# Kernel optimization log

Measured on AMD Instinct MI355X. Metric: run time of the kernel, lower is better.

## Reference

```python
import jax, jax.numpy as jnp
import numpy as np

B, GNN_DIM, TR_DIM, F = 16384, 512, 768, 1024


def setup_inputs() -> dict:
    key = jax.random.key(0)
    ks = jax.random.split(key, 16)
    s = 0.02
    return {
        "gnn_features": jax.random.normal(ks[0], (B, GNN_DIM), jnp.float32),
        "transformer_features": jax.random.normal(ks[1], (B, TR_DIM), jnp.float32),
        # gnn_projector / transformer_projector (torch Linear: y = x @ W.T + b)
        "Wg": jax.random.normal(ks[2], (F, GNN_DIM), jnp.float32) * s,
        "bg": jnp.zeros((F,), jnp.float32),
        "Wt": jax.random.normal(ks[3], (F, TR_DIM), jnp.float32) * s,
        "bt": jnp.zeros((F,), jnp.float32),
        # MultiheadAttention value-projection slice of in_proj_weight and out_proj.
        # With seq_len==1 the softmax over a single key is identically 1, so the
        # attention output is exactly out_proj(v_proj(key)); Q/K projections do
        # not affect the output (their gradients are exactly zero).
        "Wv": jax.random.normal(ks[4], (F, F), jnp.float32) * s,
        "bv": jnp.zeros((F,), jnp.float32),
        "Wo": jax.random.normal(ks[5], (F, F), jnp.float32) * s,
        "bo": jnp.zeros((F,), jnp.float32),
        # fusion_layers: Linear(2F -> F), GELU, Dropout(eval: identity), Linear(F -> F)
        "W1": jax.random.normal(ks[6], (F, 2 * F), jnp.float32) * s,
        "b1": jnp.zeros((F,), jnp.float32),
        "W2": jax.random.normal(ks[7], (F, F), jnp.float32) * s,
        "b2": jnp.zeros((F,), jnp.float32),
    }


def reference(gnn_features, transformer_features, Wg, bg, Wt, bt, Wv, bv, Wo, bo, W1, b1, W2, b2):
    # projections to fusion space  [B, F]
    gnn_proj = gnn_features @ Wg.T + bg
    tr_proj = transformer_features @ Wt.T + bt
    # degenerate single-token cross-attention: softmax over 1 key == 1, so
    # attn(q, k, v=k) = out_proj(v_proj(k)) regardless of the query.
    gnn_attended = (tr_proj @ Wv.T + bv) @ Wo.T + bo   # attention(gnn_seq, tr_seq, tr_seq)
    tr_attended = (gnn_proj @ Wv.T + bv) @ Wo.T + bo   # attention(tr_seq, gnn_seq, gnn_seq)
    combined = jnp.concatenate([gnn_attended, tr_attended], axis=-1)  # [B, 2F]
    h = jax.nn.gelu(combined @ W1.T + b1, approximate=False)          # exact GELU (torch default)
    fused = h @ W2.T + b2
    return fused + gnn_proj + tr_proj
```

## Files before the change

kernel.cpp:

```cpp
#include <hip/hip_runtime.h>
#include <cmath>

#define GAS __attribute__((address_space(1)))
#define LAS __attribute__((address_space(3)))

typedef __bf16 bf16x8 __attribute__((ext_vector_type(8)));
typedef float f32x4 __attribute__((ext_vector_type(4)));
typedef float f32x16 __attribute__((ext_vector_type(16)));

__device__ __forceinline__ void gload16(const void* g, void* l) {
    __builtin_amdgcn_global_load_lds((const GAS void*)g, (LAS void*)l, 16, 0, 0);
}

__global__ void k_prep(const float* __restrict__ gnn, const float* __restrict__ tr,
                       const float* __restrict__ Wo, const float* __restrict__ W1,
                       const float* __restrict__ W2, const float* __restrict__ Wg,
                       const float* __restrict__ Wt, const float* __restrict__ Wv,
                       __bf16* __restrict__ X, __bf16* __restrict__ W1ab,
                       __bf16* __restrict__ Wp, __bf16* __restrict__ Wv_b,
                       __bf16* __restrict__ WoT, __bf16* __restrict__ WgT,
                       __bf16* __restrict__ WtT) {
    __shared__ float t[32][33];
    int b = blockIdx.x;
    int tid = threadIdx.x;
    if (b < 12928) {
        const float* src; __bf16* dst; int sld, dld, base, c8;
        if (b < 4096)       { src=gnn;     sld=512;  dst=X+1024;         dld=2304; base=0;     c8=64; }
        else if (b < 10240) { src=tr;      sld=768;  dst=X+1536;         dld=2304; base=4096;  c8=96; }
        else if (b < 10752) { src=W1;      sld=2048; dst=W1ab;           dld=1024; base=10240; c8=128; }
        else if (b < 11264) { src=W1+1024; sld=2048; dst=W1ab+1024*1024; dld=1024; base=10752; c8=128; }
        else if (b < 11776) { src=W2;      sld=1024; dst=Wp;             dld=2304; base=11264; c8=128; }
        else if (b < 12032) { src=Wg;      sld=512;  dst=Wp+1024;        dld=2304; base=11776; c8=64; }
        else if (b < 12416) { src=Wt;      sld=768;  dst=Wp+1536;       dld=2304; base=12032; c8=96; }
        else                { src=Wv;      sld=1024; dst=Wv_b;           dld=1024; base=12416; c8=128; }
        int idx = (b - base) * 256 + tid;
        int r = idx / c8;
        int c = (idx - r * c8) << 3;
        const float4* s = reinterpret_cast<const float4*>(src + (long)r * sld + c);
        float4 x0 = s[0], x1 = s[1];
        bf16x8 v;
        v[0]=(__bf16)x0.x; v[1]=(__bf16)x0.y; v[2]=(__bf16)x0.z; v[3]=(__bf16)x0.w;
        v[4]=(__bf16)x1.x; v[5]=(__bf16)x1.y; v[6]=(__bf16)x1.z; v[7]=(__bf16)x1.w;
        *reinterpret_cast<bf16x8*>(dst + (long)r * dld + c) = v;
    } else {
        int bb = b - 12928;
        const float* src; __bf16* dst; int R, C, tile;
        if (bb < 1024)      { src=Wo; dst=WoT; R=1024; C=1024; tile=bb; }
        else if (bb < 1536) { src=Wg; dst=WgT; R=1024; C=512;  tile=bb-1024; }
        else                { src=Wt; dst=WtT; R=1024; C=768;  tile=bb-1536; }
        int tx_n = C >> 5;
        int c0 = (tile % tx_n) << 5, r0 = (tile / tx_n) << 5;
        int tx = tid & 31, ty = tid >> 5;
        #pragma unroll
        for (int i = 0; i < 32; i += 8)
            t[ty + i][tx] = src[(long)(r0 + ty + i) * C + c0 + tx];
        __syncthreads();
        #pragma unroll
        for (int i = 0; i < 32; i += 8)
            dst[(long)(c0 + ty + i) * R + r0 + tx] = (__bf16)t[tx][ty + i];
    }
}

__global__ void k_bias1(const float* __restrict__ Wo, const float* __restrict__ bv,
                        const float* __restrict__ bo, const float* __restrict__ Wv,
                        const float* __restrict__ bt, const float* __restrict__ bg,
                        float* __restrict__ b_att, float* __restrict__ vb_t,
                        float* __restrict__ vb_g) {
    int b = blockIdx.x;
    const float* mat; const float* vec; float* dst; int i; bool addbo = false;
    if (b < 1024)      { mat = Wo; vec = bv; dst = b_att; i = b;        addbo = true; }
    else if (b < 2048) { mat = Wv; vec = bt; dst = vb_t;  i = b - 1024; }
    else               { mat = Wv; vec = bg; dst = vb_g;  i = b - 2048; }
    float s = 0.f;
    for (int k = threadIdx.x; k < 1024; k += 256) s += mat[(long)i * 1024 + k] * vec[k];
    __shared__ float red[256];
    red[threadIdx.x] = s;
    __syncthreads();
    for (int off = 128; off > 0; off >>= 1) {
        if (threadIdx.x < off) red[threadIdx.x] += red[threadIdx.x + off];
        __syncthreads();
    }
    if (threadIdx.x == 0) dst[i] = red[0] + (addbo ? bo[i] : 0.f);
}

__global__ void k_bias_z2(const float* __restrict__ W1, const float* __restrict__ b_att,
                          const float* __restrict__ b1, const __bf16* __restrict__ U12,
                          const float* __restrict__ vb_t, const float* __restrict__ vb_g,
                          const float* __restrict__ bt, const float* __restrict__ bg,
                          const float* __restrict__ b2,
                          float* __restrict__ bz2, float* __restrict__ b_out) {
    int i = blockIdx.x;
    float s = 0.f;
    for (int k = threadIdx.x; k < 1024; k += 256) {
        s += (W1[(long)i * 2048 + k] + W1[(long)i * 2048 + 1024 + k]) * b_att[k];
        s += (float)U12[(long)i * 1024 + k] * vb_t[k];
        s += (float)U12[(long)(i + 1024) * 1024 + k] * vb_g[k];
    }
    __shared__ float red[256];
    red[threadIdx.x] = s;
    __syncthreads();
    for (int off = 128; off > 0; off >>= 1) {
        if (threadIdx.x < off) red[threadIdx.x] += red[threadIdx.x + off];
        __syncthreads();
    }
    if (threadIdx.x == 0) {
        bz2[i] = red[0] + b1[i];
        b_out[i] = b2[i] + bg[i] + bt[i];
    }
}

__device__ __forceinline__ void gemm64_body(
    const __bf16* __restrict__ A, int lda,
    const __bf16* __restrict__ B, int ldb,
    __bf16* __restrict__ C, int ldc,
    int K, int n_tiles, int bid) {
    constexpr int BM = 64, BN = 64, BK = 32;
    constexpr int MR = 2, NR = 2;
    __shared__ alignas(16) __bf16 As[2][BM][BK];
    __shared__ alignas(16) __bf16 Bs[2][BN][BK];

    const int tid = threadIdx.x;
    const int lane = tid & 63;
    const int wave = tid >> 6;
    const int bn = bid % n_tiles;
    const int bm = bid / n_tiles;
    const int m0 = bm * BM, n0 = bn * BN;

    const int rp_l = tid >> 2;
    const int sp = tid & 3;
    const int wr = (wave >> 1) * 32;
    const int wc = (wave & 1) * 32;
    const int fr = lane & 15;
    const int fb = (lane >> 4) << 4;

    f32x4 acc[MR][NR] = {};
    const int nk = K / BK;

    auto stage = [&](int buf, int kt) {
        int rl = (rp_l & ~1) | ((rp_l ^ (rp_l >> 2)) & 1);
        int sl = sp ^ (rl & 3);
        gload16(A + (long)(m0 + rl) * lda + kt * BK + sl * 8, (char*)&As[buf][0][0] + tid * 16);
        gload16(B + (long)(n0 + rl) * ldb + kt * BK + sl * 8, (char*)&Bs[buf][0][0] + tid * 16);
    };

    stage(0, 0);
    for (int kt = 0; kt < nk; ++kt) {
        const int buf = kt & 1;
        __syncthreads();
        if (kt + 1 < nk) stage(buf ^ 1, kt + 1);
        const char* abase = (const char*)&As[buf][0][0];
        const char* bbase = (const char*)&Bs[buf][0][0];
        bf16x8 af[MR], bfr[NR];
        #pragma unroll
        for (int m = 0; m < MR; ++m) {
            int r = wr + m * 16 + fr;
            af[m] = *(const bf16x8*)(abase + (((r << 6) + fb) ^ ((r & 7) << 4)));
        }
        #pragma unroll
        for (int n = 0; n < NR; ++n) {
            int r = wc + n * 16 + fr;
            bfr[n] = *(const bf16x8*)(bbase + (((r << 6) + fb) ^ ((r & 7) << 4)));
        }
        #pragma unroll
        for (int m = 0; m < MR; ++m)
            #pragma unroll
            for (int n = 0; n < NR; ++n)
                acc[m][n] = __builtin_amdgcn_mfma_f32_16x16x32_bf16(af[m], bfr[n], acc[m][n], 0, 0, 0);
    }

    const int r0 = (lane >> 4) << 2;
    #pragma unroll
    for (int n = 0; n < NR; ++n) {
        const int gc = n0 + wc + n * 16 + fr;
        #pragma unroll
        for (int m = 0; m < MR; ++m) {
            const long rbase = (long)(m0 + wr + m * 16 + r0);
            #pragma unroll
            for (int r = 0; r < 4; ++r)
                C[(rbase + r) * ldc + gc] = (__bf16)acc[m][n][r];
        }
    }
}

__global__ __launch_bounds__(256, 2) void k_gemmL1(
    const __bf16* __restrict__ W1ab, const __bf16* __restrict__ WoT,
    const __bf16* __restrict__ WtT, const __bf16* __restrict__ WgT,
    const __bf16* __restrict__ Wv_b, __bf16* __restrict__ U12,
    __bf16* __restrict__ VtT, __bf16* __restrict__ VgT) {
    int b = blockIdx.x;
    if (b < 512)      gemm64_body(W1ab, 1024, WoT, 1024, U12, 1024, 1024, 16, b);
    else if (b < 704) gemm64_body(WtT, 1024, Wv_b, 1024, VtT, 1024, 1024, 16, b - 512);
    else              gemm64_body(WgT, 1024, Wv_b, 1024, VgT, 1024, 1024, 16, b - 704);
}

__global__ __launch_bounds__(256, 2) void k_gemmL2(
    const __bf16* __restrict__ U12, const __bf16* __restrict__ VtT,
    const __bf16* __restrict__ VgT, __bf16* __restrict__ M1) {
    int b = blockIdx.x;
    if (b < 192) gemm64_body(U12, 1024, VtT, 1024, M1 + 512, 1280, 1024, 12, b);
    else         gemm64_body(U12 + 1024 * 1024, 1024, VgT, 1024, M1, 1280, 1024, 8, b - 192);
}

template <int MODE>
__device__ __forceinline__ void gemm8_body(
    const __bf16* __restrict__ A, int lda,
    const __bf16* __restrict__ B, int ldb,
    void* __restrict__ Cv, int ldc,
    const float* __restrict__ bias,
    int K, int n_tiles) {
    __shared__ char lds[131072];

    const int tid = threadIdx.x;
    const int lane = tid & 63;
    const int wave = tid >> 6;
    const int wm = wave >> 2;
    const int wn = wave & 3;

    int bid = blockIdx.x;
    const int nwg = gridDim.x;
    if ((nwg & 7) == 0) bid = (bid & 7) * (nwg >> 3) + (bid >> 3);
    const int bn = bid % n_tiles;
    const int bm = bid / n_tiles;
    const int m0 = bm * 256, n0 = bn * 256;

    const int rowA = ((tid >> 7) << 4) + (tid & 15);
    const int colA = (((tid >> 6) & 1) << 5) + (((tid >> 4) & 3) << 3);
    const int rowB = ((tid >> 6) << 4) + (tid & 15);
    const int colB = (((tid >> 4) & 3) << 3);
    const __bf16* Ag = A + (long)(m0 + rowA) * lda + colA;
    const __bf16* Bg = B + (long)(n0 + rowB) * ldb + colB;
    const int tid16 = tid * 16;

    const int laneA = ((lane >> 4) & 1) * 2048 + (lane >> 5) * 256 + (lane & 15) * 16;
    const int laneB = ((lane >> 4) & 1) * 1024 + (lane >> 5) * 256 + (lane & 15) * 16;
    const int bnh = wn >> 1;
    const int bno = (wn & 1) * 4096;

    f32x16 acc[4][2] = {};
    bf16x8 af[2][2];
    bf16x8 bfr[2][2][2];

    const int nk = K >> 6;
    const int NI = nk >> 1;

#define STAGE_A(PAR, KT, MH, QH) \
    gload16(Ag + (long)(KT) * 64 + (long)((MH) * 128 + (QH) * 64) * lda, \
            lds + (PAR) * 32768 + (MH) * 16384 + (QH) * 8192 + tid16)
#define STAGE_B(PAR, KT, NH, KK) \
    gload16(Bg + (long)(KT) * 64 + (KK) * 32 + (long)((NH) * 128) * ldb, \
            lds + 65536 + (PAR) * 32768 + (NH) * 16384 + (KK) * 8192 + tid16)
#define VMC6 asm volatile("s_waitcnt vmcnt(6)" ::: "memory")
#define VMC0 asm volatile("s_waitcnt vmcnt(0)" ::: "memory")
#define BAR  __builtin_amdgcn_s_barrier()
#define LGKM0 asm volatile("s_waitcnt lgkmcnt(0)" ::: "memory")
#define RD_A32(PAR, QH, KK) { \
        const char* a_ = lds + (PAR) * 32768 + wm * 16384 + (QH) * 8192 + (KK) * 1024; \
        _Pragma("unroll") \
        for (int fm_ = 0; fm_ < 2; ++fm_) { \
            _Pragma("unroll") \
            for (int h_ = 0; h_ < 2; ++h_) \
                af[fm_][h_] = *(const bf16x8*)(a_ + fm_ * 4096 + h_ * 512 + laneA); } }
#define RD_B32(KK, PAR) { \
        const char* b_ = lds + 65536 + (PAR) * 32768 + bnh * 16384 + (KK) * 8192 + bno; \
        _Pragma("unroll") \
        for (int fn_ = 0; fn_ < 2; ++fn_) { \
            _Pragma("unroll") \
            for (int h_ = 0; h_ < 2; ++h_) \
                bfr[KK][h_][fn_] = *(const bf16x8*)(b_ + fn_ * 2048 + h_ * 512 + laneB); } }
#define MFMA8(QH, KK) { \
        __builtin_amdgcn_s_setprio(1); \
        _Pragma("unroll") \
        for (int h_ = 0; h_ < 2; ++h_) { \
            _Pragma("unroll") \
            for (int fm_ = 0; fm_ < 2; ++fm_) { \
                _Pragma("unroll") \
                for (int fn_ = 0; fn_ < 2; ++fn_) \
                    acc[(QH) * 2 + fm_][fn_] = __builtin_amdgcn_mfma_f32_32x32x16_bf16( \
                        af[fm_][h_], bfr[KK][h_][fn_], acc[(QH) * 2 + fm_][fn_], 0, 0, 0); } } \
        __builtin_amdgcn_s_setprio(0); }

    STAGE_A(0, 0, 0, 0); STAGE_A(0, 0, 1, 0);
    STAGE_B(0, 0, 0, 0); STAGE_B(0, 0, 1, 0);
    STAGE_B(0, 0, 0, 1); STAGE_B(0, 0, 1, 1);
    STAGE_A(0, 0, 0, 1); STAGE_A(0, 0, 1, 1);
    STAGE_A(1, 1, 0, 0); STAGE_A(1, 1, 1, 0);
    STAGE_B(1, 1, 0, 0); STAGE_B(1, 1, 1, 0);
    STAGE_B(1, 1, 0, 1); STAGE_B(1, 1, 1, 1);
    VMC6;
    BAR;

    for (int I = 0; I < NI; ++I) {
        const int t = 2 * I;
        const bool nl = (I + 1 < NI);
        RD_B32(0, 0); RD_A32(0, 0, 0);
        STAGE_A(1, t + 1, 0, 1); STAGE_A(1, t + 1, 1, 1);
        BAR; LGKM0; MFMA8(0, 0); BAR;
        RD_B32(1, 0); RD_A32(0, 0, 1);
        if (nl) { STAGE_B(0, t + 2, 0, 0); STAGE_B(0, t + 2, 1, 0); }
        BAR; LGKM0; MFMA8(0, 1); BAR;
        RD_A32(0, 1, 0);
        if (nl) { STAGE_A(0, t + 2, 0, 0); STAGE_A(0, t + 2, 1, 0); }
        BAR; LGKM0; MFMA8(1, 0); BAR;
        RD_A32(0, 1, 1);
        if (nl) { STAGE_B(0, t + 2, 0, 1); STAGE_B(0, t + 2, 1, 1); VMC6; } else { VMC0; }
        BAR; LGKM0; MFMA8(1, 1); BAR;
        RD_B32(0, 1); RD_A32(1, 0, 0);
        if (nl) { STAGE_A(0, t + 2, 0, 1); STAGE_A(0, t + 2, 1, 1); }
        BAR; LGKM0; MFMA8(0, 0); BAR;
        RD_B32(1, 1); RD_A32(1, 0, 1);
        if (nl) { STAGE_B(1, t + 3, 0, 0); STAGE_B(1, t + 3, 1, 0); }
        BAR; LGKM0; MFMA8(0, 1); BAR;
        RD_A32(1, 1, 0);
        if (nl) { STAGE_A(1, t + 3, 0, 0); STAGE_A(1, t + 3, 1, 0); }
        BAR; LGKM0; MFMA8(1, 0); BAR;
        RD_A32(1, 1, 1);
        if (nl) { STAGE_B(1, t + 3, 0, 1); STAGE_B(1, t + 3, 1, 1); VMC6; }
        BAR; LGKM0; MFMA8(1, 1); BAR;
    }
#undef MFMA8
#undef RD_B32
#undef RD_A32
#undef LGKM0
#undef BAR
#undef VMC0
#undef VMC6
#undef STAGE_B
#undef STAGE_A

    char* scr = lds + wave * 16384;
    const int col32 = lane & 31;
    const int rb5 = (lane >> 5) << 2;
    float bval[2];
    bval[0] = bias ? bias[n0 + wn * 64 + col32] : 0.0f;
    bval[1] = bias ? bias[n0 + wn * 64 + 32 + col32] : 0.0f;

    #pragma unroll
    for (int FM = 0; FM < 4; ++FM) {
        #pragma unroll
        for (int fn_ = 0; fn_ < 2; ++fn_) {
            #pragma unroll
            for (int rg = 0; rg < 16; ++rg) {
                float v = acc[FM][fn_][rg] + bval[fn_];
                if (MODE == 1) {
                    float u = v * (0.7978845608f + 0.0356774081f * v * v);
                    float e = __expf(-2.0f * fabsf(u));
                    float th = (1.0f - e) / (1.0f + e);
                    th = copysignf(th, u);
                    v = 0.5f * v * (1.0f + th);
                }
                int srow = (rg & 3) + ((rg >> 2) << 3) + rb5;
                *(float*)(scr + srow * 272 + (fn_ * 32 + col32) * 4) = v;
            }
        }
        asm volatile("s_waitcnt lgkmcnt(0)" ::: "memory");
        if (MODE == 2) {
            #pragma unroll
            for (int rep = 0; rep < 8; ++rep) {
                int row = rep * 4 + (lane >> 4);
                f32x4 val = *(const f32x4*)(scr + row * 272 + (lane & 15) * 16);
                long grow = (long)(m0 + wm * 128 + FM * 32 + row);
                *(f32x4*)&((float*)Cv)[grow * ldc + n0 + wn * 64 + (lane & 15) * 4] = val;
            }
        } else {
            #pragma unroll
            for (int rep = 0; rep < 4; ++rep) {
                int row = rep * 8 + (lane >> 3);
                f32x4 v0 = *(const f32x4*)(scr + row * 272 + (lane & 7) * 32);
                f32x4 v1 = *(const f32x4*)(scr + row * 272 + (lane & 7) * 32 + 16);
                bf16x8 o;
                o[0] = (__bf16)v0[0]; o[1] = (__bf16)v0[1]; o[2] = (__bf16)v0[2]; o[3] = (__bf16)v0[3];
                o[4] = (__bf16)v1[0]; o[5] = (__bf16)v1[1]; o[6] = (__bf16)v1[2]; o[7] = (__bf16)v1[3];
                long grow = (long)(m0 + wm * 128 + FM * 32 + row);
                *(bf16x8*)&((__bf16*)Cv)[grow * ldc + n0 + wn * 64 + (lane & 7) * 8] = o;
            }
        }
        asm volatile("s_waitcnt lgkmcnt(0)" ::: "memory");
    }
}

__global__ __launch_bounds__(512, 2) void k_g256_gelu(
    const __bf16* __restrict__ A, int lda, const __bf16* __restrict__ B, int ldb,
    void* __restrict__ Cv, int ldc, const float* __restrict__ bias, int K, int n_tiles) {
    gemm8_body<1>(A, lda, B, ldb, Cv, ldc, bias, K, n_tiles);
}
__global__ __launch_bounds__(512, 2) void k_g256_out(
    const __bf16* __restrict__ A, int lda, const __bf16* __restrict__ B, int ldb,
    void* __restrict__ Cv, int ldc, const float* __restrict__ bias, int K, int n_tiles) {
    gemm8_body<2>(A, lda, B, ldb, Cv, ldc, bias, K, n_tiles);
}

extern "C" void kernel_launch(void* const* d_in, const int* in_sizes, int n_in,
                              void* d_out, int out_size, void* d_ws, size_t ws_size,
                              hipStream_t stream) {
    constexpr int Bsz = 16384, F = 1024, GD = 512, TD = 768;
    constexpr int XLD = F + GD + TD;

    const float* gnn = (const float*)d_in[0];
    const float* tr  = (const float*)d_in[1];
    const float* Wg  = (const float*)d_in[2];
    const float* bg  = (const float*)d_in[3];
    const float* Wt  = (const float*)d_in[4];
    const float* bt  = (const float*)d_in[5];
    const float* Wv  = (const float*)d_in[6];
    const float* bv  = (const float*)d_in[7];
    const float* Wo  = (const float*)d_in[8];
    const float* bo  = (const float*)d_in[9];
    const float* W1  = (const float*)d_in[10];
    const float* b1  = (const float*)d_in[11];
    const float* W2  = (const float*)d_in[12];
    const float* b2  = (const float*)d_in[13];
    float* out = (float*)d_out;

    char* w = (char*)d_ws;
    auto alloc = [&](size_t bytes) {
        char* p = w;
        w += (bytes + 255) & ~(size_t)255;
        return p;
    };
    __bf16* X    = (__bf16*)alloc((size_t)Bsz * XLD * 2);
    __bf16* M1   = (__bf16*)alloc((size_t)F * (GD + TD) * 2);
    __bf16* Wp   = (__bf16*)alloc((size_t)F * XLD * 2);
    __bf16* W1ab = (__bf16*)alloc((size_t)2 * F * F * 2);
    __bf16* Wv_b = (__bf16*)alloc((size_t)F * F * 2);
    __bf16* WoT  = (__bf16*)alloc((size_t)F * F * 2);
    __bf16* WgT  = (__bf16*)alloc((size_t)GD * F * 2);
    __bf16* WtT  = (__bf16*)alloc((size_t)TD * F * 2);
    __bf16* U12  = (__bf16*)alloc((size_t)2 * F * F * 2);
    __bf16* VtT  = (__bf16*)alloc((size_t)TD * F * 2);
    __bf16* VgT  = (__bf16*)alloc((size_t)GD * F * 2);
    float* b_att = (float*)alloc(F * 4);
    float* vb_t  = (float*)alloc(F * 4);
    float* vb_g  = (float*)alloc(F * 4);
    float* bz2   = (float*)alloc(F * 4);
    float* b_out = (float*)alloc(F * 4);
    if ((size_t)(w - (char*)d_ws) > ws_size) return;

    dim3 b256(256);

    k_prep<<<dim3(15232), b256, 0, stream>>>(gnn, tr, Wo, W1, W2, Wg, Wt, Wv,
                                             X, W1ab, Wp, Wv_b, WoT, WgT, WtT);
    k_bias1<<<dim3(3072), b256, 0, stream>>>(Wo, bv, bo, Wv, bt, bg, b_att, vb_t, vb_g);

    k_gemmL1<<<dim3(832), b256, 0, stream>>>(W1ab, WoT, WtT, WgT, Wv_b, U12, VtT, VgT);

    k_bias_z2<<<dim3(F), b256, 0, stream>>>(W1, b_att, b1, U12, vb_t, vb_g, bt, bg, b2,
                                            bz2, b_out);

    k_gemmL2<<<dim3(320), b256, 0, stream>>>(U12, VtT, VgT, M1);

    k_g256_gelu<<<dim3((Bsz / 256) * (F / 256)), dim3(512), 0, stream>>>(
        X + F, XLD, M1, GD + TD, X, XLD, bz2, GD + TD, F / 256);

    k_g256_out<<<dim3((Bsz / 256) * (F / 256)), dim3(512), 0, stream>>>(
        X, XLD, Wp, XLD, out, F, b_out, XLD, F / 256);
}
```

Baseline: 217.1 us.

## Fold bias kernel into prep and enlarge weight-precompute GEMM tiles to 128x128

```diff
diff --git a/kernel.cpp b/kernel.cpp
--- a/kernel.cpp
+++ b/kernel.cpp
@@ -16,10 +16,14 @@
                        const float* __restrict__ Wo, const float* __restrict__ W1,
                        const float* __restrict__ W2, const float* __restrict__ Wg,
                        const float* __restrict__ Wt, const float* __restrict__ Wv,
+                       const float* __restrict__ bv, const float* __restrict__ bo,
+                       const float* __restrict__ bt, const float* __restrict__ bg,
                        __bf16* __restrict__ X, __bf16* __restrict__ W1ab,
                        __bf16* __restrict__ Wp, __bf16* __restrict__ Wv_b,
                        __bf16* __restrict__ WoT, __bf16* __restrict__ WgT,
-                       __bf16* __restrict__ WtT) {
+                       __bf16* __restrict__ WtT,
+                       float* __restrict__ b_att, float* __restrict__ vb_t,
+                       float* __restrict__ vb_g) {
     __shared__ float t[32][33];
     int b = blockIdx.x;
     int tid = threadIdx.x;
@@ -31,7 +35,7 @@
         else if (b < 11264) { src=W1+1024; sld=2048; dst=W1ab+1024*1024; dld=1024; base=10752; c8=128; }
         else if (b < 11776) { src=W2;      sld=1024; dst=Wp;             dld=2304; base=11264; c8=128; }
         else if (b < 12032) { src=Wg;      sld=512;  dst=Wp+1024;        dld=2304; base=11776; c8=64; }
-        else if (b < 12416) { src=Wt;      sld=768;  dst=Wp+1536;       dld=2304; base=12032; c8=96; }
+        else if (b < 12416) { src=Wt;      sld=768;  dst=Wp+1536;        dld=2304; base=12032; c8=96; }
         else                { src=Wv;      sld=1024; dst=Wv_b;           dld=1024; base=12416; c8=128; }
         int idx = (b - base) * 256 + tid;
         int r = idx / c8;
@@ -42,7 +46,7 @@
         v[0]=(__bf16)x0.x; v[1]=(__bf16)x0.y; v[2]=(__bf16)x0.z; v[3]=(__bf16)x0.w;
         v[4]=(__bf16)x1.x; v[5]=(__bf16)x1.y; v[6]=(__bf16)x1.z; v[7]=(__bf16)x1.w;
         *reinterpret_cast<bf16x8*>(dst + (long)r * dld + c) = v;
-    } else {
+    } else if (b < 15232) {
         int bb = b - 12928;
         const float* src; __bf16* dst; int R, C, tile;
         if (bb < 1024)      { src=Wo; dst=WoT; R=1024; C=1024; tile=bb; }
@@ -58,29 +62,23 @@
         #pragma unroll
         for (int i = 0; i < 32; i += 8)
             dst[(long)(c0 + ty + i) * R + r0 + tx] = (__bf16)t[tx][ty + i];
-    }
-}
-
-__global__ void k_bias1(const float* __restrict__ Wo, const float* __restrict__ bv,
-                        const float* __restrict__ bo, const float* __restrict__ Wv,
-                        const float* __restrict__ bt, const float* __restrict__ bg,
-                        float* __restrict__ b_att, float* __restrict__ vb_t,
-                        float* __restrict__ vb_g) {
-    int b = blockIdx.x;
-    const float* mat; const float* vec; float* dst; int i; bool addbo = false;
-    if (b < 1024)      { mat = Wo; vec = bv; dst = b_att; i = b;        addbo = true; }
-    else if (b < 2048) { mat = Wv; vec = bt; dst = vb_t;  i = b - 1024; }
-    else               { mat = Wv; vec = bg; dst = vb_g;  i = b - 2048; }
-    float s = 0.f;
-    for (int k = threadIdx.x; k < 1024; k += 256) s += mat[(long)i * 1024 + k] * vec[k];
-    __shared__ float red[256];
-    red[threadIdx.x] = s;
-    __syncthreads();
-    for (int off = 128; off > 0; off >>= 1) {
-        if (threadIdx.x < off) red[threadIdx.x] += red[threadIdx.x + off];
+    } else {
+        int bb = b - 15232;
+        const float* mat; const float* vec; float* dst; int i; bool addbo = false;
+        if (bb < 1024)      { mat = Wo; vec = bv; dst = b_att; i = bb;        addbo = true; }
+        else if (bb < 2048) { mat = Wv; vec = bt; dst = vb_t;  i = bb - 1024; }
+        else                { mat = Wv; vec = bg; dst = vb_g;  i = bb - 2048; }
+        float s = 0.f;
+        for (int k = tid; k < 1024; k += 256) s += mat[(long)i * 1024 + k] * vec[k];
+        float* red = &t[0][0];
+        red[tid] = s;
         __syncthreads();
-    }
-    if (threadIdx.x == 0) dst[i] = red[0] + (addbo ? bo[i] : 0.f);
+        for (int off = 128; off > 0; off >>= 1) {
+            if (tid < off) red[tid] += red[tid + off];
+            __syncthreads();
+        }
+        if (tid == 0) dst[i] = red[0] + (addbo ? bo[i] : 0.f);
+    }
 }
 
 __global__ void k_bias_z2(const float* __restrict__ W1, const float* __restrict__ b_att,
@@ -109,38 +107,42 @@
     }
 }
 
-__device__ __forceinline__ void gemm64_body(
+template <int MODE>
+__device__ __forceinline__ void gemm128_body(
+    char* lds,
     const __bf16* __restrict__ A, int lda,
     const __bf16* __restrict__ B, int ldb,
-    __bf16* __restrict__ C, int ldc,
+    void* __restrict__ Cv, int ldc,
     int K, int n_tiles, int bid) {
-    constexpr int BM = 64, BN = 64, BK = 32;
-    constexpr int MR = 2, NR = 2;
-    __shared__ alignas(16) __bf16 As[2][BM][BK];
-    __shared__ alignas(16) __bf16 Bs[2][BN][BK];
-
     const int tid = threadIdx.x;
     const int lane = tid & 63;
     const int wave = tid >> 6;
+    const int wm = wave >> 1;
+    const int wn = wave & 1;
+
     const int bn = bid % n_tiles;
     const int bm = bid / n_tiles;
-    const int m0 = bm * BM, n0 = bn * BN;
-
-    const int rp_l = tid >> 2;
-    const int sp = tid & 3;
-    const int wr = (wave >> 1) * 32;
-    const int wc = (wave & 1) * 32;
+    const int m0 = bm * 128, n0 = bn * 128;
+
+    const int rowS = ((tid >> 6) << 4) + (tid & 15);
+    const int colS = ((tid >> 4) & 3) << 3;
+    const __bf16* Ag = A + (long)(m0 + rowS) * lda + colS;
+    const __bf16* Bg = B + (long)(n0 + rowS) * ldb + colS;
+    const long lda64 = (long)64 * lda;
+    const long ldb64 = (long)64 * ldb;
+    const int tid16 = tid * 16;
+    const int l16 = lane * 16;
     const int fr = lane & 15;
-    const int fb = (lane >> 4) << 4;
-
-    f32x4 acc[MR][NR] = {};
-    const int nk = K / BK;
+
+    f32x4 acc[4][4] = {};
+    const int nk = K >> 5;
 
     auto stage = [&](int buf, int kt) {
-        int rl = (rp_l & ~1) | ((rp_l ^ (rp_l >> 2)) & 1);
-        int sl = sp ^ (rl & 3);
-        gload16(A + (long)(m0 + rl) * lda + kt * BK + sl * 8, (char*)&As[buf][0][0] + tid * 16);
-        gload16(B + (long)(n0 + rl) * ldb + kt * BK + sl * 8, (char*)&Bs[buf][0][0] + tid * 16);
+        const long ko = (long)kt * 32;
+        gload16(Ag + ko,         lds + buf * 8192 + tid16);
+        gload16(Ag + ko + lda64, lds + buf * 8192 + 4096 + tid16);
+        gload16(Bg + ko,         lds + 16384 + buf * 8192 + tid16);
+        gload16(Bg + ko + ldb64, lds + 16384 + buf * 8192 + 4096 + tid16);
     };
 
     stage(0, 0);
@@ -148,57 +150,80 @@
         const int buf = kt & 1;
         __syncthreads();
         if (kt + 1 < nk) stage(buf ^ 1, kt + 1);
-        const char* abase = (const char*)&As[buf][0][0];
-        const char* bbase = (const char*)&Bs[buf][0][0];
-        bf16x8 af[MR], bfr[NR];
-        #pragma unroll
-        for (int m = 0; m < MR; ++m) {
-            int r = wr + m * 16 + fr;
-            af[m] = *(const bf16x8*)(abase + (((r << 6) + fb) ^ ((r & 7) << 4)));
+        const char* a_ = lds + buf * 8192 + (wm * 4) * 1024;
+        const char* b_ = lds + 16384 + buf * 8192 + (wn * 4) * 1024;
+        bf16x8 af[4], bfr[4];
+        #pragma unroll
+        for (int m = 0; m < 4; ++m) af[m] = *(const bf16x8*)(a_ + m * 1024 + l16);
+        #pragma unroll
+        for (int n = 0; n < 4; ++n) bfr[n] = *(const bf16x8*)(b_ + n * 1024 + l16);
+        __builtin_amdgcn_s_setprio(1);
+        #pragma unroll
+        for (int m = 0; m < 4; ++m)
+            #pragma unroll
+            for (int n = 0; n < 4; ++n)
+                acc[m][n] = __builtin_amdgcn_mfma_f32_16x16x32_bf16(af[m], bfr[n], acc[m][n], 0, 0, 0);
+        __builtin_amdgcn_s_setprio(0);
+    }
+    __syncthreads();
+
+    char* scr = lds + wave * 4352;
+    const int r0q = (lane >> 4) << 2;
+    #pragma unroll
+    for (int mq = 0; mq < 4; ++mq) {
+        #pragma unroll
+        for (int n_ = 0; n_ < 4; ++n_) {
+            #pragma unroll
+            for (int r = 0; r < 4; ++r) {
+                float v = acc[mq][n_][r];
+                *(float*)(scr + (r0q + r) * 272 + (n_ * 16 + fr) * 4) = v;
+            }
         }
-        #pragma unroll
-        for (int n = 0; n < NR; ++n) {
-            int r = wc + n * 16 + fr;
-            bfr[n] = *(const bf16x8*)(bbase + (((r << 6) + fb) ^ ((r & 7) << 4)));
+        asm volatile("s_waitcnt lgkmcnt(0)" ::: "memory");
+        if (MODE == 2) {
+            #pragma unroll
+            for (int rep = 0; rep < 4; ++rep) {
+                int row = rep * 4 + (lane >> 4);
+                f32x4 val = *(const f32x4*)(scr + row * 272 + (lane & 15) * 16);
+                long grow = (long)(m0 + wm * 64 + mq * 16 + row);
+                *(f32x4*)&((float*)Cv)[grow * ldc + n0 + wn * 64 + (lane & 15) * 4] = val;
+            }
+        } else {
+            #pragma unroll
+            for (int rep = 0; rep < 2; ++rep) {
+                int row = rep * 8 + (lane >> 3);
+                f32x4 v0 = *(const f32x4*)(scr + row * 272 + (lane & 7) * 32);
+                f32x4 v1 = *(const f32x4*)(scr + row * 272 + (lane & 7) * 32 + 16);
+                bf16x8 o;
+                o[0] = (__bf16)v0[0]; o[1] = (__bf16)v0[1]; o[2] = (__bf16)v0[2]; o[3] = (__bf16)v0[3];
+                o[4] = (__bf16)v1[0]; o[5] = (__bf16)v1[1]; o[6] = (__bf16)v1[2]; o[7] = (__bf16)v1[3];
+                long grow = (long)(m0 + wm * 64 + mq * 16 + row);
+                *(bf16x8*)&((__bf16*)Cv)[grow * ldc + n0 + wn * 64 + (lane & 7) * 8] = o;
+            }
         }
-        #pragma unroll
-        for (int m = 0; m < MR; ++m)
-            #pragma unroll
-            for (int n = 0; n < NR; ++n)
-                acc[m][n] = __builtin_amdgcn_mfma_f32_16x16x32_bf16(af[m], bfr[n], acc[m][n], 0, 0, 0);
-    }
-
-    const int r0 = (lane >> 4) << 2;
-    #pragma unroll
-    for (int n = 0; n < NR; ++n) {
-        const int gc = n0 + wc + n * 16 + fr;
-        #pragma unroll
-        for (int m = 0; m < MR; ++m) {
-            const long rbase = (long)(m0 + wr + m * 16 + r0);
-            #pragma unroll
-            for (int r = 0; r < 4; ++r)
-                C[(rbase + r) * ldc + gc] = (__bf16)acc[m][n][r];
-        }
-    }
-}
-
-__global__ __launch_bounds__(256, 2) void k_gemmL1(
+        asm volatile("s_waitcnt lgkmcnt(0)" ::: "memory");
+    }
+}
+
+__global__ __launch_bounds__(256, 4) void k_gemmL1(
     const __bf16* __restrict__ W1ab, const __bf16* __restrict__ WoT,
     const __bf16* __restrict__ WtT, const __bf16* __restrict__ WgT,
     const __bf16* __restrict__ Wv_b, __bf16* __restrict__ U12,
     __bf16* __restrict__ VtT, __bf16* __restrict__ VgT) {
+    __shared__ char lds[32768];
     int b = blockIdx.x;
-    if (b < 512)      gemm64_body(W1ab, 1024, WoT, 1024, U12, 1024, 1024, 16, b);
-    else if (b < 704) gemm64_body(WtT, 1024, Wv_b, 1024, VtT, 1024, 1024, 16, b - 512);
-    else              gemm64_body(WgT, 1024, Wv_b, 1024, VgT, 1024, 1024, 16, b - 704);
-}
-
-__global__ __launch_bounds__(256, 2) void k_gemmL2(
+    if (b < 128)      gemm128_body<0>(lds, W1ab, 1024, WoT, 1024, U12, 1024, 1024, 8, b);
+    else if (b < 176) gemm128_body<0>(lds, WtT, 1024, Wv_b, 1024, VtT, 1024, 1024, 8, b - 128);
+    else              gemm128_body<0>(lds, WgT, 1024, Wv_b, 1024, VgT, 1024, 1024, 8, b - 176);
+}
+
+__global__ __launch_bounds__(256, 4) void k_gemmL2(
     const __bf16* __restrict__ U12, const __bf16* __restrict__ VtT,
     const __bf16* __restrict__ VgT, __bf16* __restrict__ M1) {
+    __shared__ char lds[32768];
     int b = blockIdx.x;
-    if (b < 192) gemm64_body(U12, 1024, VtT, 1024, M1 + 512, 1280, 1024, 12, b);
-    else         gemm64_body(U12 + 1024 * 1024, 1024, VgT, 1024, M1, 1280, 1024, 8, b - 192);
+    if (b < 48) gemm128_body<0>(lds, U12, 1024, VtT, 1024, M1 + 512, 1280, 1024, 6, b);
+    else        gemm128_body<0>(lds, U12 + 1024 * 1024, 1024, VgT, 1024, M1, 1280, 1024, 4, b - 48);
 }
 
 template <int MODE>
@@ -437,16 +462,17 @@
 
     dim3 b256(256);
 
-    k_prep<<<dim3(15232), b256, 0, stream>>>(gnn, tr, Wo, W1, W2, Wg, Wt, Wv,
-                                             X, W1ab, Wp, Wv_b, WoT, WgT, WtT);
-    k_bias1<<<dim3(3072), b256, 0, stream>>>(Wo, bv, bo, Wv, bt, bg, b_att, vb_t, vb_g);
-
-    k_gemmL1<<<dim3(832), b256, 0, stream>>>(W1ab, WoT, WtT, WgT, Wv_b, U12, VtT, VgT);
+    k_prep<<<dim3(18304), b256, 0, stream>>>(gnn, tr, Wo, W1, W2, Wg, Wt, Wv,
+                                             bv, bo, bt, bg,
+                                             X, W1ab, Wp, Wv_b, WoT, WgT, WtT,
+                                             b_att, vb_t, vb_g);
+
+    k_gemmL1<<<dim3(208), b256, 0, stream>>>(W1ab, WoT, WtT, WgT, Wv_b, U12, VtT, VgT);
 
     k_bias_z2<<<dim3(F), b256, 0, stream>>>(W1, b_att, b1, U12, vb_t, vb_g, bt, bg, b2,
                                             bz2, b_out);
 
-    k_gemmL2<<<dim3(320), b256, 0, stream>>>(U12, VtT, VgT, M1);
+    k_gemmL2<<<dim3(80), b256, 0, stream>>>(U12, VtT, VgT, M1);
 
     k_g256_gelu<<<dim3((Bsz / 256) * (F / 256)), dim3(512), 0, stream>>>(
         X + F, XLD, M1, GD + TD, X, XLD, bz2, GD + TD, F / 256);
```

After: 221.6 us. 2.1% more time.
